# Kernel optimization log

Measured on AMD Instinct MI355X. Metric: run time of the kernel, lower is better.

## Reference

```python
import jax, jax.numpy as jnp
import numpy as np

NH = 16   # num heads
CS = 16   # inner chunk size

def _gelu(x):
    return jax.nn.gelu(x, approximate=True)

def _diff_gelu(x):
    t = jnp.tanh(0.79788456 * x * (1.0 + 0.044715 * x * x))
    return 0.5 * x * ((1.0 - t * t) * (0.79788456 + 0.1070322243 * x * x)) + 0.5 * (1.0 + t)

def _ln_fused_l2_bwd(x, tgt, gamma, beta, eps=1e-6):
    # x, tgt: [B*nh, CS, f]; gamma/beta: [1, nh, 1, f]
    Bnh, N, HF = x.shape
    mu = x.mean(-1, keepdims=True)
    var = x.var(-1, keepdims=True)
    std = jnp.sqrt(var + eps)
    x_hat = (x - mu) / std
    y = gamma * x_hat.reshape(-1, NH, N, HF) + beta
    go = y - tgt.reshape(-1, NH, N, HF)
    gxh = (go * gamma).reshape(Bnh, N, HF)
    return (HF * gxh - gxh.sum(-1, keepdims=True) - x_hat * (gxh * x_hat).sum(-1, keepdims=True)) / (HF * std)

def setup_inputs() -> dict:
    key = jax.random.key(0)
    ks = jax.random.split(key, 8)
    B, nh, f, hf4, n_chunks = 4, NH, 64, 256, 128
    Bnh = B * nh
    XQ = jax.random.normal(ks[0], (n_chunks, Bnh, CS, f), jnp.float32)
    XK = jax.random.normal(ks[1], (n_chunks, Bnh, CS, f), jnp.float32)
    XV = jax.random.normal(ks[2], (n_chunks, Bnh, CS, f), jnp.float32)
    # inner-loop lr coeffs (ilr * token_idx ~ lr/head_dim): small positive
    coeff = jax.random.uniform(ks[3], (n_chunks, Bnh, CS, 1), jnp.float32) * 0.01
    coeff_last = jax.random.uniform(ks[4], (n_chunks, Bnh, 1, 1), jnp.float32) * 0.01
    W1 = jax.random.normal(ks[5], (Bnh, f, hf4), jnp.float32) * 0.02
    b1 = jnp.zeros((Bnh, 1, hf4), jnp.float32)
    W2 = jax.random.normal(ks[6], (Bnh, hf4, f), jnp.float32) * 0.02
    b2 = jnp.zeros((Bnh, 1, f), jnp.float32)
    ln_weight = jnp.ones((1, nh, 1, f), jnp.float32)
    ln_bias = jnp.zeros((1, nh, 1, f), jnp.float32)
    return dict(XQ=XQ, XK=XK, XV=XV, coeff=coeff, coeff_last=coeff_last,
                W1=W1, b1=b1, W2=W2, b2=b2, ln_weight=ln_weight, ln_bias=ln_bias)

def reference(XQ, XK, XV, coeff, coeff_last, W1, b1, W2, b2, ln_weight, ln_bias):
    n_chunks, Bnh, _, f = XQ.shape
    attn_b = jnp.tril(jnp.ones((CS, CS), XQ.dtype))

    def step(carry, inp):
        W1c, b1c, W2c, b2c = carry
        xv, xk, xq, c, cl = inp
        Z1 = xk @ W1c + b1c                      # [Bnh, CS, 4f]
        X2 = _gelu(Z1)
        Z2 = X2 @ W2c + b2c                      # [Bnh, CS, f]
        dZ2 = _ln_fused_l2_bwd(Z2, xv - xk, ln_weight, ln_bias)
        dZ1 = (dZ2 @ W2c.transpose(0, 2, 1)) * _diff_gelu(Z1)
        b1_bar = b1c - c * (attn_b @ dZ1)
        A1 = jnp.tril(xq @ xk.transpose(0, 2, 1))
        Z1_bar = xq @ W1c - c * (A1 @ dZ1) + b1_bar
        X2_bar = _gelu(Z1_bar)
        b2_bar = b2c - c * (attn_b @ dZ2)
        A2 = jnp.tril(X2_bar @ X2.transpose(0, 2, 1))
        Z2_bar = X2_bar @ W2c - c * (A2 @ dZ2) + b2_bar
        W1n = W1c - cl * (xk.transpose(0, 2, 1) @ dZ1)
        W2n = W2c - cl * (X2.transpose(0, 2, 1) @ dZ2)
        return (W1n, b1_bar[:, -1:], W2n, b2_bar[:, -1:]), Z2_bar

    _, Z2_all = jax.lax.scan(step, (W1, b1, W2, b2), (XV, XK, XQ, coeff, coeff_last))
    # [n_chunks, Bnh, CS, f] -> [Bnh, N, f]
    return Z2_all.transpose(1, 0, 2, 3).reshape(Bnh, n_chunks * CS, f)
```

## Files before the change

kernel.cpp:

```cpp
#include <hip/hip_runtime.h>

typedef __attribute__((ext_vector_type(8))) short bf16x8;
typedef __attribute__((ext_vector_type(4))) float f32x4;
typedef __attribute__((ext_vector_type(2))) unsigned int u32x2;

#define MFMA16(a,b,c) __builtin_amdgcn_mfma_f32_16x16x32_bf16(a,b,c,0,0,0)
#define A_GELU 0.7978845608028654f

#define OFF_W1B   0u
#define OFF_W2F   36864u
#define OFF_XK    70656u
#define OFF_XQ    72960u
#define OFF_X2    75264u
#define OFF_X2B   83712u
#define OFF_DZ2B  92160u
#define OFF_DZ1CT 94464u
#define OFF_DZ2CT 114944u
#define OFF_XKCT  120064u
#define OFF_X2CT  125184u
#define OFF_M1    145664u
#define OFF_M2    146944u
#define OFF_Z2F   148224u
#define OFF_Z2G   152576u
#define OFF_TGT   156928u
#define OFF_B2    161024u
#define OFF_COEF  161536u
#define OFF_CL    161600u
#define SMEM_BYTES 161616u

#define W2COL(col, row) ((col) ^ (((row)&7)<<3))

__device__ __forceinline__ float fast_tanh(float u){
    float e = __expf(2.0f*u);
    return 1.0f - 2.0f/(e + 1.0f);
}
__device__ __forceinline__ float gelu_f(float x){
    float t = fast_tanh(A_GELU*(x + 0.044715f*x*x*x));
    return 0.5f*x*(1.0f+t);
}
__device__ __forceinline__ float dgelu_f(float x){
    float x2 = x*x;
    float t = fast_tanh(A_GELU*x*(1.0f + 0.044715f*x2));
    return 0.5f*x*((1.0f-t*t)*(A_GELU + 0.1070322243f*x2)) + 0.5f*(1.0f+t);
}
__device__ __forceinline__ short f2bf(float f){
    unsigned u = __builtin_bit_cast(unsigned, f);
    u += 0x7FFFu + ((u >> 16) & 1u);
    return (short)(u >> 16);
}
__device__ __forceinline__ float bf2f(unsigned short s){
    unsigned u = ((unsigned)s) << 16;
    return __builtin_bit_cast(float, u);
}
__device__ __forceinline__ unsigned pkbf(float a, float b){
    unsigned r;
    asm("v_cvt_pk_bf16_f32 %0, %1, %2" : "=v"(r) : "v"(a), "v"(b));
    return r;
}
__device__ __forceinline__ bf16x8 ldfrag(const unsigned short* p){
    return *(const bf16x8*)p;
}

__global__ __launch_bounds__(512, 1)
void ttt_m2(const float* __restrict__ XQ, const float* __restrict__ XK,
            const float* __restrict__ XV, const float* __restrict__ coeff,
            const float* __restrict__ coeff_last,
            const float* __restrict__ W1g, const float* __restrict__ b1g,
            const float* __restrict__ W2g, const float* __restrict__ b2g,
            const float* __restrict__ gammag, const float* __restrict__ betag,
            float* __restrict__ out)
{
    const int h  = blockIdx.x;
    const int t  = threadIdx.x;
    const int l  = t & 63;
    const int w  = t >> 6;
    const int lo = l & 15;
    const int hi = l >> 4;

    extern __shared__ char smem[];
    unsigned short* sW1bu  = (unsigned short*)(smem + OFF_W1B);
    unsigned short* sW2fu  = (unsigned short*)(smem + OFF_W2F);
    unsigned short* sxku   = (unsigned short*)(smem + OFF_XK);
    unsigned short* sxqu   = (unsigned short*)(smem + OFF_XQ);
    unsigned short* sX2u   = (unsigned short*)(smem + OFF_X2);
    unsigned short* sX2bu  = (unsigned short*)(smem + OFF_X2B);
    unsigned short* sdZ2bu = (unsigned short*)(smem + OFF_DZ2B);
    unsigned short* sdZ1ct = (unsigned short*)(smem + OFF_DZ1CT);
    unsigned short* sdZ2ct = (unsigned short*)(smem + OFF_DZ2CT);
    unsigned short* sxkct  = (unsigned short*)(smem + OFF_XKCT);
    unsigned short* sX2ct  = (unsigned short*)(smem + OFF_X2CT);
    unsigned short* sM1u   = (unsigned short*)(smem + OFF_M1);
    unsigned short* sM2u   = (unsigned short*)(smem + OFF_M2);
    float* sZ2f  = (float*)(smem + OFF_Z2F);
    float* sZ2g  = (float*)(smem + OFF_Z2G);
    float* stgt  = (float*)(smem + OFF_TGT);
    float* b2f   = (float*)(smem + OFF_B2);
    float* scoef = (float*)(smem + OFF_COEF);
    float* sCL   = (float*)(smem + OFF_CL);

    const int base1 = h*16384;
    const int base2 = h*16384;

    float mW1[4][2][4];
    float mW2[2][4][4];
    #pragma unroll
    for (int mt = 0; mt < 4; ++mt)
      #pragma unroll
      for (int tix = 0; tix < 2; ++tix)
        #pragma unroll
        for (int reg = 0; reg < 4; ++reg) {
            const int m = mt*16 + hi*4 + reg, n = (2*w + tix)*16 + lo;
            mW1[mt][tix][reg] = W1g[base1 + m*256 + n];
        }
    #pragma unroll
    for (int mi = 0; mi < 2; ++mi)
      #pragma unroll
      for (int nt = 0; nt < 4; ++nt)
        #pragma unroll
        for (int reg = 0; reg < 4; ++reg) {
            const int m = (2*w + mi)*16 + hi*4 + reg, n = nt*16 + lo;
            mW2[mi][nt][reg] = W2g[base2 + m*64 + n];
        }
    float b1reg[2];
    b1reg[0] = b1g[h*256 + (2*w)*16 + lo];
    b1reg[1] = b1g[h*256 + (2*w+1)*16 + lo];

    for (int i = 0; i < 32; ++i) {
        const int idx = i*512 + t;
        const int m = idx >> 8, n = idx & 255;
        sW1bu[n*72 + m] = f2bf(W1g[base1 + idx]);
    }
    for (int i = 0; i < 32; ++i) {
        const int idx = i*512 + t;
        const int hf = idx >> 6, f = idx & 63;
        sW2fu[f*264 + W2COL(hf, f)] = f2bf(W2g[base2 + idx]);
    }
    if (t < 64) b2f[t] = b2g[h*64 + t];
    if (t < 256) {
        for (int k = 16; k < 40; ++k) { sdZ1ct[t*40 + k] = 0; sX2ct[t*40 + k] = 0; }
    }
    if (t < 64) {
        for (int k = 16; k < 40; ++k) { sdZ2ct[t*40 + k] = 0; sxkct[t*40 + k] = 0; }
    }
    if (t < 16) {
        for (int k = 16; k < 40; ++k) { sM1u[t*40 + k] = 0; sM2u[t*40 + k] = 0; }
    }

    const float gj = gammag[(h & 15)*64 + l];
    const float bj = betag [(h & 15)*64 + l];
    __syncthreads();

    for (int ci = 0; ci < 128; ++ci) {
        const int cb = ci*65536 + h*1024;

        {
            const int r0 = w*2;
            const float xk0 = XK[cb + r0*64 + l],     xq0 = XQ[cb + r0*64 + l];
            const float xk1 = XK[cb + (r0+1)*64 + l], xq1 = XQ[cb + (r0+1)*64 + l];
            const float xv0 = XV[cb + r0*64 + l],     xv1 = XV[cb + (r0+1)*64 + l];
            const unsigned pkk = pkbf(xk0, xk1);
            const unsigned pkq = pkbf(xq0, xq1);
            sxku[r0*72 + l]     = (unsigned short)pkk;
            sxku[(r0+1)*72 + l] = (unsigned short)(pkk >> 16);
            sxqu[r0*72 + l]     = (unsigned short)pkq;
            sxqu[(r0+1)*72 + l] = (unsigned short)(pkq >> 16);
            *(unsigned*)&sxkct[l*40 + r0] = pkk;
            stgt[r0*64 + l]     = xv0 - xk0;
            stgt[(r0+1)*64 + l] = xv1 - xk1;
        }
        if (t < 16)  scoef[t] = coeff[ci*1024 + h*16 + t];
        if (t == 16) sCL[0]   = coeff_last[ci*64 + h];
        __syncthreads();
        const float clv = sCL[0];
        const float c15 = scoef[15];

        float z1s[8];
        bf16x8 afk0 = ldfrag(sxku + lo*72 + hi*8);
        bf16x8 afk1 = ldfrag(sxku + lo*72 + 32 + hi*8);
        #pragma unroll
        for (int tix = 0; tix < 2; ++tix) {
            const int n = (2*w + tix)*16 + lo;
            f32x4 acc = {b1reg[tix], b1reg[tix], b1reg[tix], b1reg[tix]};
            acc = MFMA16(afk0, ldfrag(sW1bu + n*72 + hi*8), acc);
            acc = MFMA16(afk1, ldfrag(sW1bu + n*72 + 32 + hi*8), acc);
            float g[4];
            #pragma unroll
            for (int reg = 0; reg < 4; ++reg) {
                z1s[tix*4 + reg] = acc[reg];
                g[reg] = gelu_f(acc[reg]);
            }
            const unsigned p01 = pkbf(g[0], g[1]), p23 = pkbf(g[2], g[3]);
            sX2u[(hi*4+0)*264 + n] = (unsigned short)p01;
            sX2u[(hi*4+1)*264 + n] = (unsigned short)(p01 >> 16);
            sX2u[(hi*4+2)*264 + n] = (unsigned short)p23;
            sX2u[(hi*4+3)*264 + n] = (unsigned short)(p23 >> 16);
            *(u32x2*)&sX2ct[n*40 + hi*4] = (u32x2){p01, p23};
        }
        if (w == 0) {
            bf16x8 aq0 = ldfrag(sxqu + lo*72 + hi*8);
            bf16x8 aq1 = ldfrag(sxqu + lo*72 + 32 + hi*8);
            f32x4 a1 = {0.f, 0.f, 0.f, 0.f};
            a1 = MFMA16(aq0, afk0, a1);
            a1 = MFMA16(aq1, afk1, a1);
            #pragma unroll
            for (int reg = 0; reg < 4; ++reg) {
                const int r = hi*4 + reg;
                const float cr = scoef[r];
                const float v = (lo <= r) ? (-cr*(a1[reg] + 1.0f)) : 0.0f;
                sM1u[r*40 + lo] = f2bf(v);
            }
        }
        __syncthreads();

        const int tile = w & 3, kh = w >> 2;
        const int nf = tile*16 + lo;
        {
            f32x4 accPB;
            if (kh == 0) {
                const float b2v = b2f[(ci & 1)*64 + nf];
                accPB = (f32x4){b2v, b2v, b2v, b2v};
            } else accPB = (f32x4){0.f, 0.f, 0.f, 0.f};
            #pragma unroll
            for (int s = 0; s < 4; ++s) {
                const int k = (kh*4 + s)*32 + hi*8;
                accPB = MFMA16(ldfrag(sX2u + lo*264 + k),
                               ldfrag(sW2fu + nf*264 + W2COL(k, nf)), accPB);
            }
            float* dst = (kh == 0) ? sZ2g : sZ2f;
            #pragma unroll
            for (int reg = 0; reg < 4; ++reg)
                dst[(hi*4 + reg)*68 + nf] = accPB[reg];
        }
        __syncthreads();

        {
            float dzp[2];
            #pragma unroll
            for (int i = 0; i < 2; ++i) {
                const int r = w*2 + i;
                const float z2 = sZ2f[r*68 + l] + sZ2g[r*68 + l];
                float s1 = z2, s2 = z2*z2;
                #pragma unroll
                for (int m = 1; m < 64; m <<= 1) { s1 += __shfl_xor(s1, m); s2 += __shfl_xor(s2, m); }
                const float mu   = s1*(1.0f/64.0f);
                const float var  = s2*(1.0f/64.0f) - mu*mu;
                const float rstd = rsqrtf(var + 1e-6f);
                const float xh   = (z2 - mu)*rstd;
                const float go   = gj*xh + bj - stgt[r*64 + l];
                const float gg   = go*gj;
                float u1 = gg, u2 = gg*xh;
                #pragma unroll
                for (int m = 1; m < 64; m <<= 1) { u1 += __shfl_xor(u1, m); u2 += __shfl_xor(u2, m); }
                dzp[i] = (64.0f*gg - u1 - xh*u2)*(rstd*(1.0f/64.0f));
            }
            const unsigned pk = pkbf(dzp[0], dzp[1]);
            sdZ2bu[(w*2)*72 + l]   = (unsigned short)pk;
            sdZ2bu[(w*2+1)*72 + l] = (unsigned short)(pk >> 16);
            *(unsigned*)&sdZ2ct[l*40 + w*2] = pk;
        }
        __syncthreads();

        float b1old[2];
        {
            bf16x8 ad0 = ldfrag(sdZ2bu + lo*72 + hi*8);
            bf16x8 ad1 = ldfrag(sdZ2bu + lo*72 + 32 + hi*8);
            #pragma unroll
            for (int tix = 0; tix < 2; ++tix) {
                const int n = (2*w + tix)*16 + lo;
                f32x4 acc = {0.f, 0.f, 0.f, 0.f};
                bf16x8 bw;
                #pragma unroll
                for (int j = 0; j < 8; ++j)
                    bw[j] = (short)sW2fu[(hi*8 + j)*264 + (n ^ (j<<3))];
                acc = MFMA16(ad0, bw, acc);
                #pragma unroll
                for (int j = 0; j < 8; ++j)
                    bw[j] = (short)sW2fu[(32 + hi*8 + j)*264 + (n ^ (j<<3))];
                acc = MFMA16(ad1, bw, acc);
                float dv[4];
                float cs = 0.f;
                #pragma unroll
                for (int reg = 0; reg < 4; ++reg) {
                    dv[reg] = acc[reg]*dgelu_f(z1s[tix*4 + reg]);
                    cs += dv[reg];
                }
                *(u32x2*)&sdZ1ct[n*40 + hi*4] =
                    (u32x2){pkbf(dv[0], dv[1]), pkbf(dv[2], dv[3])};
                cs += __shfl_xor(cs, 16);
                cs += __shfl_xor(cs, 32);
                b1old[tix] = b1reg[tix];
                b1reg[tix] -= c15*cs;
            }
        }
        __syncthreads();

        {
            bf16x8 aq0 = ldfrag(sxqu + lo*72 + hi*8);
            bf16x8 aq1 = ldfrag(sxqu + lo*72 + 32 + hi*8);
            bf16x8 am1 = ldfrag(sM1u + lo*40 + hi*8);
            #pragma unroll
            for (int tix = 0; tix < 2; ++tix) {
                const int n = (2*w + tix)*16 + lo;
                f32x4 acc = {b1old[tix], b1old[tix], b1old[tix], b1old[tix]};
                acc = MFMA16(aq0, ldfrag(sW1bu + n*72 + hi*8), acc);
                acc = MFMA16(aq1, ldfrag(sW1bu + n*72 + 32 + hi*8), acc);
                acc = MFMA16(am1, ldfrag(sdZ1ct + n*40 + hi*8), acc);
                float g[4];
                #pragma unroll
                for (int reg = 0; reg < 4; ++reg) g[reg] = gelu_f(acc[reg]);
                const unsigned p01 = pkbf(g[0], g[1]), p23 = pkbf(g[2], g[3]);
                sX2bu[(hi*4+0)*264 + n] = (unsigned short)p01;
                sX2bu[(hi*4+1)*264 + n] = (unsigned short)(p01 >> 16);
                sX2bu[(hi*4+2)*264 + n] = (unsigned short)p23;
                sX2bu[(hi*4+3)*264 + n] = (unsigned short)(p23 >> 16);
            }
            bf16x8 bz0 = ldfrag(sdZ1ct + ((2*w)*16 + lo)*40 + hi*8);
            bf16x8 bz1 = ldfrag(sdZ1ct + ((2*w+1)*16 + lo)*40 + hi*8);
            #pragma unroll
            for (int mt = 0; mt < 4; ++mt) {
                bf16x8 axt = ldfrag(sxkct + (mt*16 + lo)*40 + hi*8);
                f32x4 z4 = {0.f,0.f,0.f,0.f};
                f32x4 u0 = MFMA16(axt, bz0, z4);
                f32x4 u1 = MFMA16(axt, bz1, z4);
                #pragma unroll
                for (int reg = 0; reg < 4; ++reg) {
                    mW1[mt][0][reg] -= clv*u0[reg];
                    mW1[mt][1][reg] -= clv*u1[reg];
                }
            }
        }
        __syncthreads();

        {
            bf16x8 bz2[4];
            #pragma unroll
            for (int nt = 0; nt < 4; ++nt)
                bz2[nt] = ldfrag(sdZ2ct + (nt*16 + lo)*40 + hi*8);
            #pragma unroll
            for (int mi = 0; mi < 2; ++mi) {
                bf16x8 ax2 = ldfrag(sX2ct + ((2*w + mi)*16 + lo)*40 + hi*8);
                #pragma unroll
                for (int nt = 0; nt < 4; ++nt) {
                    f32x4 z4 = {0.f,0.f,0.f,0.f};
                    f32x4 u = MFMA16(ax2, bz2[nt], z4);
                    #pragma unroll
                    for (int reg = 0; reg < 4; ++reg)
                        mW2[mi][nt][reg] -= clv*u[reg];
                }
            }
            if (w == 0) {
                f32x4 a2 = {0.f,0.f,0.f,0.f};
                #pragma unroll
                for (int ks = 0; ks < 8; ++ks) {
                    const int k = ks*32 + hi*8;
                    a2 = MFMA16(ldfrag(sX2bu + lo*264 + k),
                                ldfrag(sX2u + lo*264 + k), a2);
                }
                #pragma unroll
                for (int reg = 0; reg < 4; ++reg) {
                    const int r = hi*4 + reg;
                    const float cr = scoef[r];
                    const float v = (lo <= r) ? (-cr*(a2[reg] + 1.0f)) : 0.0f;
                    sM2u[r*40 + lo] = f2bf(v);
                }
            }
            if (w == 1) {
                float cs = 0.f;
                #pragma unroll
                for (int k = 0; k < 16; ++k) cs += bf2f(sdZ2ct[l*40 + k]);
                b2f[((ci+1) & 1)*64 + l] = b2f[(ci & 1)*64 + l] - c15*cs;
            }
        }
        __syncthreads();

        f32x4 accPF;
        if (kh == 0) {
            const float b2v = b2f[(ci & 1)*64 + nf];
            accPF = (f32x4){b2v, b2v, b2v, b2v};
        } else accPF = (f32x4){0.f, 0.f, 0.f, 0.f};
        #pragma unroll
        for (int s = 0; s < 4; ++s) {
            const int k = (kh*4 + s)*32 + hi*8;
            accPF = MFMA16(ldfrag(sX2bu + lo*264 + k),
                           ldfrag(sW2fu + nf*264 + W2COL(k, nf)), accPF);
        }
        if (kh == 0) {
            accPF = MFMA16(ldfrag(sM2u + lo*40 + hi*8),
                           ldfrag(sdZ2ct + nf*40 + hi*8), accPF);
        } else {
            #pragma unroll
            for (int reg = 0; reg < 4; ++reg)
                sZ2f[(hi*4 + reg)*68 + nf] = accPF[reg];
        }
        __syncthreads();

        if (kh == 0) {
            #pragma unroll
            for (int reg = 0; reg < 4; ++reg) {
                const int r = hi*4 + reg;
                out[h*131072 + (ci*16 + r)*64 + nf] = accPF[reg] + sZ2f[r*68 + nf];
            }
        }
        #pragma unroll
        for (int mt = 0; mt < 4; ++mt)
          #pragma unroll
          for (int tix = 0; tix < 2; ++tix) {
                const int n = (2*w + tix)*16 + lo, m0 = mt*16 + hi*4;
                *(u32x2*)&sW1bu[n*72 + m0] =
                    (u32x2){pkbf(mW1[mt][tix][0], mW1[mt][tix][1]),
                            pkbf(mW1[mt][tix][2], mW1[mt][tix][3])};
          }
        #pragma unroll
        for (int mi = 0; mi < 2; ++mi)
          #pragma unroll
          for (int nt = 0; nt < 4; ++nt) {
                const int n = nt*16 + lo, m0 = (2*w + mi)*16 + hi*4;
                *(u32x2*)&sW2fu[n*264 + (m0 ^ ((n&7)<<3))] =
                    (u32x2){pkbf(mW2[mi][nt][0], mW2[mi][nt][1]),
                            pkbf(mW2[mi][nt][2], mW2[mi][nt][3])};
          }
        __syncthreads();
    }
}

extern "C" void kernel_launch(void* const* d_in, const int* in_sizes, int n_in,
                              void* d_out, int out_size, void* d_ws, size_t ws_size,
                              hipStream_t stream) {
    const float* XQ  = (const float*)d_in[0];
    const float* XK  = (const float*)d_in[1];
    const float* XV  = (const float*)d_in[2];
    const float* cf  = (const float*)d_in[3];
    const float* cfl = (const float*)d_in[4];
    const float* W1  = (const float*)d_in[5];
    const float* b1  = (const float*)d_in[6];
    const float* W2  = (const float*)d_in[7];
    const float* b2  = (const float*)d_in[8];
    const float* gam = (const float*)d_in[9];
    const float* bet = (const float*)d_in[10];
    float* o = (float*)d_out;

    hipFuncSetAttribute((const void*)ttt_m2,
                        hipFuncAttributeMaxDynamicSharedMemorySize, SMEM_BYTES);
    ttt_m2<<<64, 512, SMEM_BYTES, stream>>>(XQ, XK, XV, cf, cfl, W1, b1, W2, b2, gam, bet, o);
}
```

Measured before the change: 1.070 ms.

## Prefetch next chunk inputs, drop transposed copies, and merge final Z2 pass into fewer barriers

Next-chunk XK/XQ/XV and coefficient loads move into registers on waves 4-7 during the current chunk. Those waves write them to shared memory while waves 0-3 compute the final Z2 output, which removes the per-chunk load-then-barrier at loop start and one sync. The transposed xk/X2 shared buffers are removed in favour of strided gathers from the row-major tiles, and the W2 XOR swizzle is dropped. The W1/W2 shared writeback moves earlier and the final output GEMM is done by four waves without a split-K reduction. This shrinks LDS usage but risks bank conflicts from the unswizzled and strided accesses, and leaves half the waves idle in the output stage.

```diff
diff --git a/kernel.cpp b/kernel.cpp
--- a/kernel.cpp
+++ b/kernel.cpp
@@ -16,19 +16,15 @@
 #define OFF_DZ2B  92160u
 #define OFF_DZ1CT 94464u
 #define OFF_DZ2CT 114944u
-#define OFF_XKCT  120064u
-#define OFF_X2CT  125184u
-#define OFF_M1    145664u
-#define OFF_M2    146944u
-#define OFF_Z2F   148224u
-#define OFF_Z2G   152576u
-#define OFF_TGT   156928u
-#define OFF_B2    161024u
-#define OFF_COEF  161536u
-#define OFF_CL    161600u
-#define SMEM_BYTES 161616u
-
-#define W2COL(col, row) ((col) ^ (((row)&7)<<3))
+#define OFF_M1    120064u
+#define OFF_M2    121344u
+#define OFF_Z2F   122624u
+#define OFF_Z2G   126976u
+#define OFF_TGT   131328u
+#define OFF_B2    135424u
+#define OFF_COEF  135936u
+#define OFF_CL    136000u
+#define SMEM_BYTES 136016u
 
 __device__ __forceinline__ float fast_tanh(float u){
     float e = __expf(2.0f*u);
@@ -87,8 +83,6 @@
     unsigned short* sdZ2bu = (unsigned short*)(smem + OFF_DZ2B);
     unsigned short* sdZ1ct = (unsigned short*)(smem + OFF_DZ1CT);
     unsigned short* sdZ2ct = (unsigned short*)(smem + OFF_DZ2CT);
-    unsigned short* sxkct  = (unsigned short*)(smem + OFF_XKCT);
-    unsigned short* sX2ct  = (unsigned short*)(smem + OFF_X2CT);
     unsigned short* sM1u   = (unsigned short*)(smem + OFF_M1);
     unsigned short* sM2u   = (unsigned short*)(smem + OFF_M2);
     float* sZ2f  = (float*)(smem + OFF_Z2F);
@@ -133,14 +127,14 @@
     for (int i = 0; i < 32; ++i) {
         const int idx = i*512 + t;
         const int hf = idx >> 6, f = idx & 63;
-        sW2fu[f*264 + W2COL(hf, f)] = f2bf(W2g[base2 + idx]);
+        sW2fu[f*264 + hf] = f2bf(W2g[base2 + idx]);
     }
     if (t < 64) b2f[t] = b2g[h*64 + t];
     if (t < 256) {
-        for (int k = 16; k < 40; ++k) { sdZ1ct[t*40 + k] = 0; sX2ct[t*40 + k] = 0; }
+        for (int k = 16; k < 40; ++k) sdZ1ct[t*40 + k] = 0;
     }
     if (t < 64) {
-        for (int k = 16; k < 40; ++k) { sdZ2ct[t*40 + k] = 0; sxkct[t*40 + k] = 0; }
+        for (int k = 16; k < 40; ++k) sdZ2ct[t*40 + k] = 0;
     }
     if (t < 16) {
         for (int k = 16; k < 40; ++k) { sM1u[t*40 + k] = 0; sM2u[t*40 + k] = 0; }
@@ -148,31 +142,46 @@
 
     const float gj = gammag[(h & 15)*64 + l];
     const float bj = betag [(h & 15)*64 + l];
+
+    {
+        const int r0 = w*2;
+        const float xk0 = XK[h*1024 + r0*64 + l],     xq0 = XQ[h*1024 + r0*64 + l];
+        const float xk1 = XK[h*1024 + (r0+1)*64 + l], xq1 = XQ[h*1024 + (r0+1)*64 + l];
+        const float xv0 = XV[h*1024 + r0*64 + l],     xv1 = XV[h*1024 + (r0+1)*64 + l];
+        const unsigned pkk = pkbf(xk0, xk1), pkq = pkbf(xq0, xq1);
+        sxku[r0*72 + l]     = (unsigned short)pkk;
+        sxku[(r0+1)*72 + l] = (unsigned short)(pkk >> 16);
+        sxqu[r0*72 + l]     = (unsigned short)pkq;
+        sxqu[(r0+1)*72 + l] = (unsigned short)(pkq >> 16);
+        stgt[r0*64 + l]     = xv0 - xk0;
+        stgt[(r0+1)*64 + l] = xv1 - xk1;
+        if (t < 16)  scoef[t] = coeff[h*16 + t];
+        if (t == 16) sCL[0]   = coeff_last[h];
+    }
     __syncthreads();
 
     for (int ci = 0; ci < 128; ++ci) {
-        const int cb = ci*65536 + h*1024;
-
-        {
-            const int r0 = w*2;
-            const float xk0 = XK[cb + r0*64 + l],     xq0 = XQ[cb + r0*64 + l];
-            const float xk1 = XK[cb + (r0+1)*64 + l], xq1 = XQ[cb + (r0+1)*64 + l];
-            const float xv0 = XV[cb + r0*64 + l],     xv1 = XV[cb + (r0+1)*64 + l];
-            const unsigned pkk = pkbf(xk0, xk1);
-            const unsigned pkq = pkbf(xq0, xq1);
-            sxku[r0*72 + l]     = (unsigned short)pkk;
-            sxku[(r0+1)*72 + l] = (unsigned short)(pkk >> 16);
-            sxqu[r0*72 + l]     = (unsigned short)pkq;
-            sxqu[(r0+1)*72 + l] = (unsigned short)(pkq >> 16);
-            *(unsigned*)&sxkct[l*40 + r0] = pkk;
-            stgt[r0*64 + l]     = xv0 - xk0;
-            stgt[(r0+1)*64 + l] = xv1 - xk1;
-        }
-        if (t < 16)  scoef[t] = coeff[ci*1024 + h*16 + t];
-        if (t == 16) sCL[0]   = coeff_last[ci*64 + h];
-        __syncthreads();
         const float clv = sCL[0];
         const float c15 = scoef[15];
+        float crs[4];
+        #pragma unroll
+        for (int reg = 0; reg < 4; ++reg) crs[reg] = scoef[hi*4 + reg];
+
+        float pxk[4], pxq[4], pxv[4];
+        float pcf = 0.f, pcl = 0.f;
+        if (w >= 4 && ci < 127) {
+            const int cb1 = (ci + 1)*65536 + h*1024;
+            const int r0 = (w - 4)*4;
+            #pragma unroll
+            for (int i = 0; i < 4; ++i) {
+                pxk[i] = XK[cb1 + (r0 + i)*64 + l];
+                pxq[i] = XQ[cb1 + (r0 + i)*64 + l];
+                pxv[i] = XV[cb1 + (r0 + i)*64 + l];
+            }
+            const int u = t - 256;
+            if (u < 16)  pcf = coeff[(ci + 1)*1024 + h*16 + u];
+            if (u == 16) pcl = coeff_last[(ci + 1)*64 + h];
+        }
 
         float z1s[8];
         bf16x8 afk0 = ldfrag(sxku + lo*72 + hi*8);
@@ -194,7 +203,6 @@
             sX2u[(hi*4+1)*264 + n] = (unsigned short)(p01 >> 16);
             sX2u[(hi*4+2)*264 + n] = (unsigned short)p23;
             sX2u[(hi*4+3)*264 + n] = (unsigned short)(p23 >> 16);
-            *(u32x2*)&sX2ct[n*40 + hi*4] = (u32x2){p01, p23};
         }
         if (w == 0) {
             bf16x8 aq0 = ldfrag(sxqu + lo*72 + hi*8);
@@ -205,31 +213,39 @@
             #pragma unroll
             for (int reg = 0; reg < 4; ++reg) {
                 const int r = hi*4 + reg;
-                const float cr = scoef[r];
-                const float v = (lo <= r) ? (-cr*(a1[reg] + 1.0f)) : 0.0f;
+                const float v = (lo <= r) ? (-crs[reg]*(a1[reg] + 1.0f)) : 0.0f;
                 sM1u[r*40 + lo] = f2bf(v);
             }
         }
+        #pragma unroll
+        for (int mi = 0; mi < 2; ++mi)
+          #pragma unroll
+          for (int nt = 0; nt < 4; ++nt) {
+                const int n = nt*16 + lo, m0 = (2*w + mi)*16 + hi*4;
+                *(u32x2*)&sW2fu[n*264 + m0] =
+                    (u32x2){pkbf(mW2[mi][nt][0], mW2[mi][nt][1]),
+                            pkbf(mW2[mi][nt][2], mW2[mi][nt][3])};
+          }
         __syncthreads();
 
         const int tile = w & 3, kh = w >> 2;
         const int nf = tile*16 + lo;
         {
-            f32x4 accPB;
+            f32x4 acc;
             if (kh == 0) {
                 const float b2v = b2f[(ci & 1)*64 + nf];
-                accPB = (f32x4){b2v, b2v, b2v, b2v};
-            } else accPB = (f32x4){0.f, 0.f, 0.f, 0.f};
+                acc = (f32x4){b2v, b2v, b2v, b2v};
+            } else acc = (f32x4){0.f, 0.f, 0.f, 0.f};
             #pragma unroll
             for (int s = 0; s < 4; ++s) {
                 const int k = (kh*4 + s)*32 + hi*8;
-                accPB = MFMA16(ldfrag(sX2u + lo*264 + k),
-                               ldfrag(sW2fu + nf*264 + W2COL(k, nf)), accPB);
+                acc = MFMA16(ldfrag(sX2u + lo*264 + k),
+                             ldfrag(sW2fu + nf*264 + k), acc);
             }
             float* dst = (kh == 0) ? sZ2g : sZ2f;
             #pragma unroll
             for (int reg = 0; reg < 4; ++reg)
-                dst[(hi*4 + reg)*68 + nf] = accPB[reg];
+                dst[(hi*4 + reg)*68 + nf] = acc[reg];
         }
         __syncthreads();
 
@@ -270,15 +286,12 @@
                 f32x4 acc = {0.f, 0.f, 0.f, 0.f};
                 bf16x8 bw;
                 #pragma unroll
-                for (int j = 0; j < 8; ++j)
-                    bw[j] = (short)sW2fu[(hi*8 + j)*264 + (n ^ (j<<3))];
+                for (int j = 0; j < 8; ++j) bw[j] = (short)sW2fu[(hi*8 + j)*264 + n];
                 acc = MFMA16(ad0, bw, acc);
                 #pragma unroll
-                for (int j = 0; j < 8; ++j)
-                    bw[j] = (short)sW2fu[(32 + hi*8 + j)*264 + (n ^ (j<<3))];
+                for (int j = 0; j < 8; ++j) bw[j] = (short)sW2fu[(32 + hi*8 + j)*264 + n];
                 acc = MFMA16(ad1, bw, acc);
-                float dv[4];
-                float cs = 0.f;
+                float dv[4], cs = 0.f;
                 #pragma unroll
                 for (int reg = 0; reg < 4; ++reg) {
                     dv[reg] = acc[reg]*dgelu_f(z1s[tix*4 + reg]);
@@ -318,7 +331,12 @@
             bf16x8 bz1 = ldfrag(sdZ1ct + ((2*w+1)*16 + lo)*40 + hi*8);
             #pragma unroll
             for (int mt = 0; mt < 4; ++mt) {
-                bf16x8 axt = ldfrag(sxkct + (mt*16 + lo)*40 + hi*8);
+                bf16x8 axt = (bf16x8){0,0,0,0,0,0,0,0};
+                if (l < 32) {
+                    #pragma unroll
+                    for (int j = 0; j < 8; ++j)
+                        axt[j] = (short)sxku[(hi*8 + j)*72 + (mt*16 + lo)];
+                }
                 f32x4 z4 = {0.f,0.f,0.f,0.f};
                 f32x4 u0 = MFMA16(axt, bz0, z4);
                 f32x4 u1 = MFMA16(axt, bz1, z4);
@@ -338,7 +356,13 @@
                 bz2[nt] = ldfrag(sdZ2ct + (nt*16 + lo)*40 + hi*8);
             #pragma unroll
             for (int mi = 0; mi < 2; ++mi) {
-                bf16x8 ax2 = ldfrag(sX2ct + ((2*w + mi)*16 + lo)*40 + hi*8);
+                const int mt = 2*w + mi;
+                bf16x8 ax2 = (bf16x8){0,0,0,0,0,0,0,0};
+                if (l < 32) {
+                    #pragma unroll
+                    for (int j = 0; j < 8; ++j)
+                        ax2[j] = (short)sX2u[(hi*8 + j)*264 + (mt*16 + lo)];
+                }
                 #pragma unroll
                 for (int nt = 0; nt < 4; ++nt) {
                     f32x4 z4 = {0.f,0.f,0.f,0.f};
@@ -359,8 +383,7 @@
                 #pragma unroll
                 for (int reg = 0; reg < 4; ++reg) {
                     const int r = hi*4 + reg;
-                    const float cr = scoef[r];
-                    const float v = (lo <= r) ? (-cr*(a2[reg] + 1.0f)) : 0.0f;
+                    const float v = (lo <= r) ? (-crs[reg]*(a2[reg] + 1.0f)) : 0.0f;
                     sM2u[r*40 + lo] = f2bf(v);
                 }
             }
@@ -368,57 +391,53 @@
                 float cs = 0.f;
                 #pragma unroll
                 for (int k = 0; k < 16; ++k) cs += bf2f(sdZ2ct[l*40 + k]);
-                b2f[((ci+1) & 1)*64 + l] = b2f[(ci & 1)*64 + l] - c15*cs;
-            }
-        }
-        __syncthreads();
-
-        f32x4 accPF;
-        if (kh == 0) {
-            const float b2v = b2f[(ci & 1)*64 + nf];
-            accPF = (f32x4){b2v, b2v, b2v, b2v};
-        } else accPF = (f32x4){0.f, 0.f, 0.f, 0.f};
-        #pragma unroll
-        for (int s = 0; s < 4; ++s) {
-            const int k = (kh*4 + s)*32 + hi*8;
-            accPF = MFMA16(ldfrag(sX2bu + lo*264 + k),
-                           ldfrag(sW2fu + nf*264 + W2COL(k, nf)), accPF);
-        }
-        if (kh == 0) {
-            accPF = MFMA16(ldfrag(sM2u + lo*40 + hi*8),
-                           ldfrag(sdZ2ct + nf*40 + hi*8), accPF);
-        } else {
+                b2f[((ci + 1) & 1)*64 + l] = b2f[(ci & 1)*64 + l] - c15*cs;
+            }
+            #pragma unroll
+            for (int mt = 0; mt < 4; ++mt)
+              #pragma unroll
+              for (int tix = 0; tix < 2; ++tix) {
+                    const int n = (2*w + tix)*16 + lo, m0 = mt*16 + hi*4;
+                    *(u32x2*)&sW1bu[n*72 + m0] =
+                        (u32x2){pkbf(mW1[mt][tix][0], mW1[mt][tix][1]),
+                                pkbf(mW1[mt][tix][2], mW1[mt][tix][3])};
+              }
+        }
+        __syncthreads();
+
+        if (w < 4) {
+            const int nf2 = w*16 + lo;
+            const float b2v = b2f[(ci & 1)*64 + nf2];
+            f32x4 acc = {b2v, b2v, b2v, b2v};
+            #pragma unroll
+            for (int s = 0; s < 8; ++s) {
+                const int k0 = s*32 + hi*8;
+                acc = MFMA16(ldfrag(sX2bu + lo*264 + k0),
+                             ldfrag(sW2fu + nf2*264 + k0), acc);
+            }
+            acc = MFMA16(ldfrag(sM2u + lo*40 + hi*8),
+                         ldfrag(sdZ2ct + nf2*40 + hi*8), acc);
             #pragma unroll
             for (int reg = 0; reg < 4; ++reg)
-                sZ2f[(hi*4 + reg)*68 + nf] = accPF[reg];
-        }
-        __syncthreads();
-
-        if (kh == 0) {
-            #pragma unroll
-            for (int reg = 0; reg < 4; ++reg) {
-                const int r = hi*4 + reg;
-                out[h*131072 + (ci*16 + r)*64 + nf] = accPF[reg] + sZ2f[r*68 + nf];
-            }
-        }
-        #pragma unroll
-        for (int mt = 0; mt < 4; ++mt)
-          #pragma unroll
-          for (int tix = 0; tix < 2; ++tix) {
-                const int n = (2*w + tix)*16 + lo, m0 = mt*16 + hi*4;
-                *(u32x2*)&sW1bu[n*72 + m0] =
-                    (u32x2){pkbf(mW1[mt][tix][0], mW1[mt][tix][1]),
-                            pkbf(mW1[mt][tix][2], mW1[mt][tix][3])};
-          }
-        #pragma unroll
-        for (int mi = 0; mi < 2; ++mi)
-          #pragma unroll
-          for (int nt = 0; nt < 4; ++nt) {
-                const int n = nt*16 + lo, m0 = (2*w + mi)*16 + hi*4;
-                *(u32x2*)&sW2fu[n*264 + (m0 ^ ((n&7)<<3))] =
-                    (u32x2){pkbf(mW2[mi][nt][0], mW2[mi][nt][1]),
-                            pkbf(mW2[mi][nt][2], mW2[mi][nt][3])};
-          }
+                out[h*131072 + (ci*16 + hi*4 + reg)*64 + nf2] = acc[reg];
+        } else if (ci < 127) {
+            const int r0 = (w - 4)*4;
+            #pragma unroll
+            for (int p = 0; p < 2; ++p) {
+                const int r = r0 + 2*p;
+                const unsigned pkk = pkbf(pxk[2*p], pxk[2*p+1]);
+                const unsigned pkq = pkbf(pxq[2*p], pxq[2*p+1]);
+                sxku[r*72 + l]     = (unsigned short)pkk;
+                sxku[(r+1)*72 + l] = (unsigned short)(pkk >> 16);
+                sxqu[r*72 + l]     = (unsigned short)pkq;
+                sxqu[(r+1)*72 + l] = (unsigned short)(pkq >> 16);
+                stgt[r*64 + l]     = pxv[2*p]   - pxk[2*p];
+                stgt[(r+1)*64 + l] = pxv[2*p+1] - pxk[2*p+1];
+            }
+            const int u = t - 256;
+            if (u < 16)  scoef[u] = pcf;
+            if (u == 16) sCL[0]   = pcl;
+        }
         __syncthreads();
     }
 }
```

New measurement: 976.4 us. 8.8% less time.
